# Kernel tuning notes

Hardware: AMD Instinct MI355X
Metric: run time of the kernel (lower is better)

The kernel has to match this reference:

```python
import jax, jax.numpy as jnp
import numpy as np

VOCAB = 50000
E = 256      # text_embed_dim
K = 512      # num_kernels
KS = 9       # kernel_size
L = 8192     # num labels
B, T = 8, 2048
PAD = KS // 2


def setup_inputs() -> dict:
    key = jax.random.key(0)
    ks = jax.random.split(key, 9)
    ids = jax.random.randint(ks[0], (B, T), 0, VOCAB)
    mask = jnp.ones((B, T), dtype=jnp.int32)  # unused by forward, kept for signature parity
    target = (jax.random.uniform(ks[1], (B, L)) < 0.01).astype(jnp.float32)
    embed_w = jax.random.normal(ks[2], (VOCAB, E), jnp.float32) * 0.02
    conv_w = jax.random.normal(ks[3], (K, E, KS), jnp.float32) * (1.0 / np.sqrt(E * KS))
    conv_b = jnp.zeros((K,), jnp.float32)
    U_w = jax.random.normal(ks[4], (L, K), jnp.float32) * (1.0 / np.sqrt(K))
    final_w = jax.random.normal(ks[5], (L, K), jnp.float32) * (1.0 / np.sqrt(K))
    final_b = jnp.zeros((L,), jnp.float32)
    return {"ids": ids, "mask": mask, "G": 0, "target": target,
            "embed_w": embed_w, "conv_w": conv_w, "conv_b": conv_b,
            "U_w": U_w, "final_w": final_w, "final_b": final_b}


def _forward(ids, embed_w, conv_w, conv_b, U_w, final_w, final_b):
    # embed + (dropout=identity in eval) -> [B, E, T]
    x = embed_w[ids].transpose(0, 2, 1)
    # same-padded Conv1d, then ReLU -> text_feats [B, T, K]
    y = jax.lax.conv_general_dilated(x, conv_w, (1,), [(PAD, PAD)],
                                     dimension_numbers=("NCH", "OIH", "NCH"))
    feats = jax.nn.relu(y + conv_b[None, :, None]).transpose(0, 2, 1)
    # label-wise attention: alpha = softmax(U.weight @ feats^T, dim=2) -> [B, L, T]
    scores = jnp.einsum("lk,btk->blt", U_w, feats)
    alpha = jax.nn.softmax(scores, axis=2)
    # attended features per label -> [B, L, K]
    attn = jnp.einsum("blt,btk->blk", alpha, feats)
    # label-wise dot with final.weight + bias -> logits [B, L]
    yhat = jnp.einsum("blk,lk->bl", attn, final_w) + final_b
    return yhat


def _bce_with_logits(yhat, target):
    # mean over all elements, numerically stable
    return jnp.mean(jnp.maximum(yhat, 0) - yhat * target + jnp.log1p(jnp.exp(-jnp.abs(yhat))))


def reference(ids, mask, G, target, embed_w, conv_w, conv_b, U_w, final_w, final_b):
    yhat = _forward(ids, embed_w, conv_w, conv_b, U_w, final_w, final_b)
    loss = _bce_with_logits(yhat, target)
    return yhat, loss
```

## Files before the change

### kernel.cpp

```cpp
#include <hip/hip_runtime.h>
#include <hip/hip_bf16.h>
#include <cstdint>

#define B_ 8
#define T_ 2048
#define E_ 256
#define K_ 512
#define KS_ 9
#define L_ 8192
#define PAD_ 4
#define TP_ (T_ + 2 * PAD_)
#define KK_ (E_ * KS_)

#define FEAT_SCALE 64.0f
#define W_SCALE 16.0f
#define INV_SS 9.765625e-4f
#define INV_SS_LOG2E 1.40888719e-3f

#define NB_EMBED ((B_ * TP_ * 64) / 256)
#define NB_WT ((K_ * KK_) / 256)
#define NB_CAST ((2 * L_ * K_ / 8) / 256)

typedef __bf16 bf16x8 __attribute__((ext_vector_type(8)));
typedef float f32x4 __attribute__((ext_vector_type(4)));
typedef float f32x16 __attribute__((ext_vector_type(16)));
typedef int i32x4 __attribute__((ext_vector_type(4)));
typedef int i32x8 __attribute__((ext_vector_type(8)));

__device__ __forceinline__ unsigned short f2bf(float f) {
  union { float f; unsigned int u; } a; a.f = f;
  unsigned int r = (a.u + 0x7FFFu + ((a.u >> 16) & 1u)) >> 16;
  return (unsigned short)r;
}

__device__ __forceinline__ unsigned char f2fp8(float v) {
  return (unsigned char)(__builtin_amdgcn_cvt_pk_fp8_f32(v, v, 0, false) & 0xFF);
}

__device__ __forceinline__ unsigned int pk4_fp8(float a, float b, float c, float d) {
  int v = __builtin_amdgcn_cvt_pk_fp8_f32(a, b, 0, false);
  v = __builtin_amdgcn_cvt_pk_fp8_f32(c, d, v, true);
  return (unsigned int)v;
}

__device__ __forceinline__ void gld_lds16(const void* g, void* l) {
  __builtin_amdgcn_global_load_lds(
      (const __attribute__((address_space(1))) unsigned int*)g,
      (__attribute__((address_space(3))) unsigned int*)l, 16, 0, 0);
}

__device__ __forceinline__ f32x4 mfma_bf16(bf16x8 a, bf16x8 b, f32x4 c) {
  return __builtin_amdgcn_mfma_f32_16x16x32_bf16(a, b, c, 0, 0, 0);
}

__device__ __forceinline__ f32x16 mfma_sc64(i32x8 a, i32x8 b, f32x16 c) {
  return __builtin_amdgcn_mfma_scale_f32_32x32x64_f8f6f4(a, b, c, 0, 0, 0, 127, 0, 127);
}

__device__ __forceinline__ int f_off(int t, int k) {
  return ((t >> 6) * 32768) + (((k >> 4) * 64 + (t & 63)) << 4) + (k & 15);
}
__device__ __forceinline__ int w_off(int l, int k) {
  return ((l >> 7) * 65536) + (((k >> 4) * 128 + (l & 127)) << 4) + (k & 15);
}

__global__ __launch_bounds__(256) void k_prep(const int* __restrict__ ids,
                                              const float* __restrict__ emb,
                                              const float* __restrict__ conv_w,
                                              const float* __restrict__ U_w,
                                              const float* __restrict__ F_w,
                                              unsigned short* __restrict__ xpad,
                                              unsigned short* __restrict__ wt,
                                              unsigned char* __restrict__ u8,
                                              unsigned char* __restrict__ f8) {
  const int bx = blockIdx.x;
  const int tid = threadIdx.x;
  if (bx < NB_EMBED) {
    int gid = bx * 256 + tid;
    int row = gid >> 6;
    int e4 = (gid & 63) << 2;
    int b = row / TP_;
    int tp = row - b * TP_;
    float4 v = make_float4(0.f, 0.f, 0.f, 0.f);
    if (tp >= PAD_ && tp < T_ + PAD_) {
      int id = ids[b * T_ + tp - PAD_];
      v = *(const float4*)(emb + (size_t)id * E_ + e4);
    }
    ushort4 o;
    o.x = f2bf(v.x); o.y = f2bf(v.y); o.z = f2bf(v.z); o.w = f2bf(v.w);
    *(ushort4*)(xpad + (size_t)row * E_ + e4) = o;
  } else if (bx < NB_EMBED + NB_WT) {
    int g = (bx - NB_EMBED) * 256 + tid;
    int k = g / KK_;
    int kk = g - k * KK_;
    int j = kk >> 8, e = kk & 255;
    wt[(size_t)k * KK_ + kk] = f2bf(conv_w[(k * E_ + e) * KS_ + j]);
  } else {
    int g = (bx - NB_EMBED - NB_WT) * 256 + tid;
    int sel = g >> 19;
    int gid = g & ((1 << 19) - 1);
    const float* src = sel ? F_w : U_w;
    unsigned char* dst = sel ? f8 : u8;
    int l = gid >> 6;
    int k0 = (gid & 63) << 3;
    const float* s = src + (size_t)l * K_ + k0;
    float4 v0 = *(const float4*)(s);
    float4 v1 = *(const float4*)(s + 4);
    uint2 o;
    o.x = pk4_fp8(v0.x * W_SCALE, v0.y * W_SCALE, v0.z * W_SCALE, v0.w * W_SCALE);
    o.y = pk4_fp8(v1.x * W_SCALE, v1.y * W_SCALE, v1.z * W_SCALE, v1.w * W_SCALE);
    *(uint2*)(dst + w_off(l, k0)) = o;
  }
}

__global__ __launch_bounds__(512, 4) void k_conv(const unsigned short* __restrict__ xpad,
                                                 const unsigned short* __restrict__ wt,
                                                 const float* __restrict__ conv_b,
                                                 unsigned char* __restrict__ feats) {
  __shared__ char At[2][16384];
  __shared__ char Bt[2][16384];
  const int tid = threadIdx.x;
  const int lane = tid & 63;
  const int q = lane >> 4, c = lane & 15;
  const int w = tid >> 6;
  const int wi = w >> 1, wj = w & 1;
  const int b = blockIdx.z;
  const int t0 = blockIdx.y * 128;
  const int n0 = blockIdx.x * 128;

  const char* xb = (const char*)(xpad + (size_t)b * TP_ * E_);
  const char* wb = (const char*)wt;

  const char* asrc[2]; const char* bsrc[2]; int ldso[2];
#pragma unroll
  for (int rnd = 0; rnd < 2; ++rnd) {
    int u = rnd * 512 + tid;
    int r = u >> 3;
    int j = (u & 7) ^ (r & 7);
    asrc[rnd] = xb + (size_t)(t0 + r) * 512 + j * 16;
    bsrc[rnd] = wb + (size_t)(n0 + r) * (KK_ * 2) + j * 16;
    ldso[rnd] = u * 16;
  }

  int offA[2][2], offB[4][2];
#pragma unroll
  for (int li = 0; li < 2; ++li) {
    int r = wi * 32 + li * 16 + c;
#pragma unroll
    for (int h = 0; h < 2; ++h) offA[li][h] = r * 128 + (((4 * h + q) ^ (r & 7)) << 4);
  }
#pragma unroll
  for (int ti = 0; ti < 4; ++ti) {
    int r = wj * 64 + ti * 16 + c;
#pragma unroll
    for (int h = 0; h < 2; ++h) offB[ti][h] = r * 128 + (((4 * h + q) ^ (r & 7)) << 4);
  }

  f32x4 acc[2][4];
  f32x4 zero = {0.f, 0.f, 0.f, 0.f};
#pragma unroll
  for (int i = 0; i < 2; ++i)
#pragma unroll
    for (int j = 0; j < 4; ++j) acc[i][j] = zero;

#pragma unroll
  for (int rnd = 0; rnd < 2; ++rnd) {
    gld_lds16(asrc[rnd], At[0] + ldso[rnd]);
    gld_lds16(bsrc[rnd], Bt[0] + ldso[rnd]);
  }

  for (int it = 0; it < 36; ++it) {
    const int bsel = it & 1;
    __syncthreads();
    if (it != 35) {
      const int kkc = (it + 1) * 64;
      const int aofs = (kkc >> 8) * 512 + (kkc & 255) * 2;
      const int bofs = kkc * 2;
#pragma unroll
      for (int rnd = 0; rnd < 2; ++rnd) {
        gld_lds16(asrc[rnd] + aofs, At[bsel ^ 1] + ldso[rnd]);
        gld_lds16(bsrc[rnd] + bofs, Bt[bsel ^ 1] + ldso[rnd]);
      }
    }
    const char* aB = At[bsel];
    const char* bB = Bt[bsel];
#pragma unroll
    for (int h = 0; h < 2; ++h) {
      bf16x8 afr[2], bfr[4];
#pragma unroll
      for (int li = 0; li < 2; ++li) afr[li] = *(const bf16x8*)(aB + offA[li][h]);
#pragma unroll
      for (int ti = 0; ti < 4; ++ti) bfr[ti] = *(const bf16x8*)(bB + offB[ti][h]);
#pragma unroll
      for (int ti = 0; ti < 4; ++ti)
#pragma unroll
        for (int li = 0; li < 2; ++li)
          acc[li][ti] = mfma_bf16(afr[li], bfr[ti], acc[li][ti]);
    }
  }

  const size_t fbase = (size_t)b * T_ * K_;
#pragma unroll
  for (int ti = 0; ti < 4; ++ti) {
    int k = n0 + wj * 64 + ti * 16 + c;
    float bias = conv_b[k];
#pragma unroll
    for (int li = 0; li < 2; ++li) {
      int tb = t0 + wi * 32 + li * 16 + q * 4;
#pragma unroll
      for (int rr = 0; rr < 4; ++rr) {
        float v = fmaxf(acc[li][ti][rr] + bias, 0.f) * FEAT_SCALE;
        int t = tb + rr;
        feats[fbase + f_off(t, k)] = f2fp8(v);
      }
    }
  }
}

__global__ __launch_bounds__(512, 2) void k_attn(const unsigned char* __restrict__ feats,
                                                 const unsigned char* __restrict__ u8,
                                                 const unsigned char* __restrict__ f8,
                                                 const float* __restrict__ final_b,
                                                 float* __restrict__ out) {
  __shared__ __align__(16) char smem[131072];
  __shared__ float red[512];
  const int tid = threadIdx.x;
  const int lane = tid & 63;
  const int q2 = lane >> 5, c32 = lane & 31;
  const int w = tid >> 6;
  const int wi = w >> 1;
  const int wj = w & 1;
  const int b = blockIdx.y;
  const int l0 = blockIdx.x * 128;

  const unsigned char* fb = feats + (size_t)b * T_ * K_;

  char* Us = smem;
  char* Ws = smem + 65536;
#pragma unroll
  for (int rr = 0; rr < 8; ++rr) {
    gld_lds16(u8 + (size_t)l0 * K_ + rr * 8192 + tid * 16, Us + rr * 8192 + tid * 16);
    gld_lds16(f8 + (size_t)l0 * K_ + rr * 8192 + tid * 16, Ws + rr * 8192 + tid * 16);
  }
  __syncthreads();

  const int arow = wi * 32 + c32;
  const int abase = q2 * 4096 + arow * 16;
  i32x8 uf[8], wf[8];
#pragma unroll
  for (int s = 0; s < 8; ++s) {
    int o0 = abase + s * 8192;
    i32x4 ul = *(const i32x4*)(Us + o0);
    i32x4 uh = *(const i32x4*)(Us + o0 + 2048);
    i32x4 wl = *(const i32x4*)(Ws + o0);
    i32x4 wh = *(const i32x4*)(Ws + o0 + 2048);
    uf[s] = __builtin_shufflevector(ul, uh, 0, 1, 2, 3, 4, 5, 6, 7);
    wf[s] = __builtin_shufflevector(wl, wh, 0, 1, 2, 3, 4, 5, 6, 7);
  }
  __syncthreads();

  char* const Fs0 = smem;
  char* const Fs1 = smem + 32768;
  const unsigned char* fsrc = fb + tid * 16;
#pragma unroll
  for (int rr = 0; rr < 4; ++rr)
    gld_lds16(fsrc + rr * 8192, Fs0 + tid * 16 + rr * 8192);

  const int brow = wj * 32 + c32;
  const int bbase = q2 * 2048 + brow * 16;

  f32x16 zc;
#pragma unroll
  for (int r = 0; r < 16; ++r) zc[r] = 0.f;

  float num[16], den[16];
#pragma unroll
  for (int r = 0; r < 16; ++r) { num[r] = 0.f; den[r] = 0.f; }

  for (int tc = 0; tc < 32; ++tc) {
    const int bsel = tc & 1;
    char* const cur = bsel ? Fs1 : Fs0;
    char* const nxt = bsel ? Fs0 : Fs1;
    __syncthreads();
    if (tc != 31) {
      const unsigned char* nsrc = fsrc + (size_t)(tc + 1) * 32768;
#pragma unroll
      for (int rr = 0; rr < 4; ++rr)
        gld_lds16(nsrc + rr * 8192, nxt + tid * 16 + rr * 8192);
    }
    f32x16 accS, accV;
    {
      i32x4 flo = *(const i32x4*)(cur + bbase);
      i32x4 fhi = *(const i32x4*)(cur + bbase + 1024);
      i32x8 fa = __builtin_shufflevector(flo, fhi, 0, 1, 2, 3, 4, 5, 6, 7);
      accS = mfma_sc64(uf[0], fa, zc);
      accV = mfma_sc64(wf[0], fa, zc);
    }
#pragma unroll
    for (int s = 1; s < 8; ++s) {
      i32x4 flo = *(const i32x4*)(cur + bbase + s * 4096);
      i32x4 fhi = *(const i32x4*)(cur + bbase + s * 4096 + 1024);
      i32x8 fa = __builtin_shufflevector(flo, fhi, 0, 1, 2, 3, 4, 5, 6, 7);
      accS = mfma_sc64(uf[s], fa, accS);
      accV = mfma_sc64(wf[s], fa, accV);
    }
#pragma unroll
    for (int r = 0; r < 16; ++r) {
      float p = __builtin_exp2f(accS[r] * INV_SS_LOG2E);
      den[r] += p;
      num[r] += p * accV[r];
    }
  }

#pragma unroll
  for (int r = 0; r < 16; ++r) {
#pragma unroll
    for (int m = 1; m < 32; m <<= 1) {
      num[r] += __shfl_xor(num[r], m, 64);
      den[r] += __shfl_xor(den[r], m, 64);
    }
  }
  if (c32 == 0) {
#pragma unroll
    for (int r = 0; r < 16; ++r) {
      int ll = wi * 32 + (r & 3) + 8 * (r >> 2) + 4 * q2;
      red[wj * 256 + ll] = num[r];
      red[wj * 256 + 128 + ll] = den[r];
    }
  }
  __syncthreads();
  if (tid < 128) {
    int l = l0 + tid;
    float n = red[tid] + red[256 + tid];
    float d = red[128 + tid] + red[384 + tid];
    out[(size_t)b * L_ + l] = (n * INV_SS) / d + final_b[l];
  }
}

__global__ __launch_bounds__(256) void k_loss(const float* __restrict__ yhat,
                                              const float* __restrict__ target,
                                              float* __restrict__ loss) {
  int gid = blockIdx.x * 256 + threadIdx.x;
  float s = 0.f;
  for (int i = gid; i < B_ * L_; i += 64 * 256) {
    float y = yhat[i], t = target[i];
    s += fmaxf(y, 0.f) - y * t + log1pf(__expf(-fabsf(y)));
  }
#pragma unroll
  for (int m = 1; m < 64; m <<= 1) s += __shfl_xor(s, m, 64);
  if ((threadIdx.x & 63) == 0) atomicAdd(loss, s * (1.0f / (B_ * L_)));
}

extern "C" void kernel_launch(void* const* d_in, const int* in_sizes, int n_in,
                              void* d_out, int out_size, void* d_ws, size_t ws_size,
                              hipStream_t stream) {
  const int* ids = (const int*)d_in[0];
  const float* target = (const float*)d_in[3];
  const float* emb = (const float*)d_in[4];
  const float* conv_w = (const float*)d_in[5];
  const float* conv_b = (const float*)d_in[6];
  const float* U_w = (const float*)d_in[7];
  const float* F_w = (const float*)d_in[8];
  const float* final_b = (const float*)d_in[9];
  float* out = (float*)d_out;

  char* ws = (char*)d_ws;
  unsigned short* xpad = (unsigned short*)ws;
  size_t off = (size_t)B_ * TP_ * E_ * 2;
  unsigned short* wt = (unsigned short*)(ws + off);
  off += (size_t)K_ * KK_ * 2;
  unsigned char* u8 = (unsigned char*)(ws + off);
  off += (size_t)L_ * K_;
  unsigned char* f8 = (unsigned char*)(ws + off);
  off += (size_t)L_ * K_;
  unsigned char* feats = (unsigned char*)(ws + off);
  off += (size_t)B_ * T_ * K_;
  if (ws_size < off) return;

  k_prep<<<dim3(NB_EMBED + NB_WT + NB_CAST), 256, 0, stream>>>(
      ids, emb, conv_w, U_w, F_w, xpad, wt, u8, f8);
  hipMemsetAsync(out + B_ * L_, 0, sizeof(float), stream);
  k_conv<<<dim3(K_ / 128, T_ / 128, B_), 512, 0, stream>>>(xpad, wt, conv_b, feats);
  k_attn<<<dim3(L_ / 128, B_), 512, 0, stream>>>(feats, u8, f8, final_b, out);
  k_loss<<<dim3(64), 256, 0, stream>>>(out, target, out + B_ * L_);
}
```

Baseline: 289.4 us.

## Rework conv GEMM to 32x32x16 MFMA with 256-thread blocks and new LDS layout

The conv GEMM kernel now uses 32x32x16 bf16 MFMA instead of 16x16x32. It runs 4 waves per block, each computing a 64x64 tile with four 32x32 accumulators, and the LDS staging is laid out k-major in 16-byte column chunks rather than XOR-swizzled rows. The fp8 weight cast in prep now writes 16-byte chunks per thread instead of 8. The attention kernel zeroes its accumulators in place rather than special-casing the first MFMA. The aim is fewer LDS reads per MFMA and wider stores. The risks are LDS bank conflicts from the new unswizzled layout and lower occupancy per block.

```diff
diff --git a/kernel.cpp b/kernel.cpp
--- a/kernel.cpp
+++ b/kernel.cpp
@@ -19,7 +19,7 @@
 
 #define NB_EMBED ((B_ * TP_ * 64) / 256)
 #define NB_WT ((K_ * KK_) / 256)
-#define NB_CAST ((2 * L_ * K_ / 8) / 256)
+#define NB_CAST 2048
 
 typedef __bf16 bf16x8 __attribute__((ext_vector_type(8)));
 typedef float f32x4 __attribute__((ext_vector_type(4)));
@@ -49,8 +49,8 @@
       (__attribute__((address_space(3))) unsigned int*)l, 16, 0, 0);
 }
 
-__device__ __forceinline__ f32x4 mfma_bf16(bf16x8 a, bf16x8 b, f32x4 c) {
-  return __builtin_amdgcn_mfma_f32_16x16x32_bf16(a, b, c, 0, 0, 0);
+__device__ __forceinline__ f32x16 mfma32_bf16(bf16x8 a, bf16x8 b, f32x16 c) {
+  return __builtin_amdgcn_mfma_f32_32x32x16_bf16(a, b, c, 0, 0, 0);
 }
 
 __device__ __forceinline__ f32x16 mfma_sc64(i32x8 a, i32x8 b, f32x16 c) {
@@ -97,33 +97,37 @@
     wt[(size_t)k * KK_ + kk] = f2bf(conv_w[(k * E_ + e) * KS_ + j]);
   } else {
     int g = (bx - NB_EMBED - NB_WT) * 256 + tid;
-    int sel = g >> 19;
-    int gid = g & ((1 << 19) - 1);
+    int sel = g >> 18;
+    int gi = g & ((1 << 18) - 1);
+    int u = (gi >> 6) & 31;
+    int l = ((gi >> 11) << 6) | (gi & 63);
     const float* src = sel ? F_w : U_w;
     unsigned char* dst = sel ? f8 : u8;
-    int l = gid >> 6;
-    int k0 = (gid & 63) << 3;
-    const float* s = src + (size_t)l * K_ + k0;
+    const float* s = src + (size_t)l * K_ + u * 16;
     float4 v0 = *(const float4*)(s);
     float4 v1 = *(const float4*)(s + 4);
-    uint2 o;
+    float4 v2 = *(const float4*)(s + 8);
+    float4 v3 = *(const float4*)(s + 12);
+    uint4 o;
     o.x = pk4_fp8(v0.x * W_SCALE, v0.y * W_SCALE, v0.z * W_SCALE, v0.w * W_SCALE);
     o.y = pk4_fp8(v1.x * W_SCALE, v1.y * W_SCALE, v1.z * W_SCALE, v1.w * W_SCALE);
-    *(uint2*)(dst + w_off(l, k0)) = o;
-  }
-}
-
-__global__ __launch_bounds__(512, 4) void k_conv(const unsigned short* __restrict__ xpad,
+    o.z = pk4_fp8(v2.x * W_SCALE, v2.y * W_SCALE, v2.z * W_SCALE, v2.w * W_SCALE);
+    o.w = pk4_fp8(v3.x * W_SCALE, v3.y * W_SCALE, v3.z * W_SCALE, v3.w * W_SCALE);
+    *(uint4*)(dst + w_off(l, u * 16)) = o;
+  }
+}
+
+__global__ __launch_bounds__(256, 2) void k_conv(const unsigned short* __restrict__ xpad,
                                                  const unsigned short* __restrict__ wt,
                                                  const float* __restrict__ conv_b,
                                                  unsigned char* __restrict__ feats) {
-  __shared__ char At[2][16384];
-  __shared__ char Bt[2][16384];
+  __shared__ __align__(16) char sm[2][32768];
   const int tid = threadIdx.x;
   const int lane = tid & 63;
-  const int q = lane >> 4, c = lane & 15;
+  const int q2 = lane >> 5, c32 = lane & 31;
   const int w = tid >> 6;
-  const int wi = w >> 1, wj = w & 1;
+  const int wt_i = w >> 1;
+  const int wn = w & 1;
   const int b = blockIdx.z;
   const int t0 = blockIdx.y * 128;
   const int n0 = blockIdx.x * 128;
@@ -131,90 +135,75 @@
   const char* xb = (const char*)(xpad + (size_t)b * TP_ * E_);
   const char* wb = (const char*)wt;
 
-  const char* asrc[2]; const char* bsrc[2]; int ldso[2];
-#pragma unroll
-  for (int rnd = 0; rnd < 2; ++rnd) {
-    int u = rnd * 512 + tid;
-    int r = u >> 3;
-    int j = (u & 7) ^ (r & 7);
-    asrc[rnd] = xb + (size_t)(t0 + r) * 512 + j * 16;
-    bsrc[rnd] = wb + (size_t)(n0 + r) * (KK_ * 2) + j * 16;
-    ldso[rnd] = u * 16;
-  }
-
-  int offA[2][2], offB[4][2];
-#pragma unroll
-  for (int li = 0; li < 2; ++li) {
-    int r = wi * 32 + li * 16 + c;
-#pragma unroll
-    for (int h = 0; h < 2; ++h) offA[li][h] = r * 128 + (((4 * h + q) ^ (r & 7)) << 4);
-  }
-#pragma unroll
-  for (int ti = 0; ti < 4; ++ti) {
-    int r = wj * 64 + ti * 16 + c;
-#pragma unroll
-    for (int h = 0; h < 2; ++h) offB[ti][h] = r * 128 + (((4 * h + q) ^ (r & 7)) << 4);
-  }
-
-  f32x4 acc[2][4];
-  f32x4 zero = {0.f, 0.f, 0.f, 0.f};
-#pragma unroll
-  for (int i = 0; i < 2; ++i)
-#pragma unroll
-    for (int j = 0; j < 4; ++j) acc[i][j] = zero;
-
-#pragma unroll
-  for (int rnd = 0; rnd < 2; ++rnd) {
-    gld_lds16(asrc[rnd], At[0] + ldso[rnd]);
-    gld_lds16(bsrc[rnd], Bt[0] + ldso[rnd]);
-  }
+  const char* aptr[4]; int au8[4];
+  const char* bptr[4];
+#pragma unroll
+  for (int r = 0; r < 4; ++r) {
+    int d = r * 4096 + tid * 16;
+    int u = d >> 11;
+    int row = (d >> 4) & 127;
+    aptr[r] = xb + (size_t)(t0 + row) * 512;
+    au8[r] = u * 8;
+    bptr[r] = wb + (size_t)(n0 + row) * (KK_ * 2) + u * 16;
+  }
+  const int ldso = tid * 16;
+
+#define STAGE(BUF, KKC)                                                    \
+  {                                                                        \
+    _Pragma("unroll") for (int r = 0; r < 4; ++r) {                        \
+      int kkg = (KKC) + au8[r];                                            \
+      int j = kkg >> 8, e0 = kkg & 255;                                    \
+      gld_lds16(aptr[r] + j * 512 + e0 * 2, (BUF) + r * 4096 + ldso);      \
+    }                                                                      \
+    _Pragma("unroll") for (int r = 0; r < 4; ++r)                          \
+      gld_lds16(bptr[r] + (KKC) * 2, (BUF) + 16384 + r * 4096 + ldso);     \
+  }
+
+  f32x16 acc00, acc01, acc10, acc11;
+#pragma unroll
+  for (int r = 0; r < 16; ++r) { acc00[r] = 0.f; acc01[r] = 0.f; acc10[r] = 0.f; acc11[r] = 0.f; }
+
+  STAGE(sm[0], 0)
+
+  const int aoff0 = (wt_i * 64 + c32) * 16;
+  const int boff0 = 16384 + (wn * 64 + c32) * 16;
 
   for (int it = 0; it < 36; ++it) {
-    const int bsel = it & 1;
     __syncthreads();
-    if (it != 35) {
-      const int kkc = (it + 1) * 64;
-      const int aofs = (kkc >> 8) * 512 + (kkc & 255) * 2;
-      const int bofs = kkc * 2;
-#pragma unroll
-      for (int rnd = 0; rnd < 2; ++rnd) {
-        gld_lds16(asrc[rnd] + aofs, At[bsel ^ 1] + ldso[rnd]);
-        gld_lds16(bsrc[rnd] + bofs, Bt[bsel ^ 1] + ldso[rnd]);
-      }
-    }
-    const char* aB = At[bsel];
-    const char* bB = Bt[bsel];
-#pragma unroll
-    for (int h = 0; h < 2; ++h) {
-      bf16x8 afr[2], bfr[4];
-#pragma unroll
-      for (int li = 0; li < 2; ++li) afr[li] = *(const bf16x8*)(aB + offA[li][h]);
-#pragma unroll
-      for (int ti = 0; ti < 4; ++ti) bfr[ti] = *(const bf16x8*)(bB + offB[ti][h]);
-#pragma unroll
-      for (int ti = 0; ti < 4; ++ti)
-#pragma unroll
-        for (int li = 0; li < 2; ++li)
-          acc[li][ti] = mfma_bf16(afr[li], bfr[ti], acc[li][ti]);
-    }
-  }
+    if (it != 35) STAGE(sm[(it + 1) & 1], (it + 1) * 64)
+    const char* buf = sm[it & 1];
+#pragma unroll
+    for (int ks = 0; ks < 4; ++ks) {
+      const char* base = buf + (ks * 2 + q2) * 2048;
+      bf16x8 a0 = *(const bf16x8*)(base + aoff0);
+      bf16x8 a1 = *(const bf16x8*)(base + aoff0 + 512);
+      bf16x8 b0 = *(const bf16x8*)(base + boff0);
+      bf16x8 b1 = *(const bf16x8*)(base + boff0 + 512);
+      acc00 = mfma32_bf16(a0, b0, acc00);
+      acc01 = mfma32_bf16(a0, b1, acc01);
+      acc10 = mfma32_bf16(a1, b0, acc10);
+      acc11 = mfma32_bf16(a1, b1, acc11);
+    }
+  }
+#undef STAGE
 
   const size_t fbase = (size_t)b * T_ * K_;
-#pragma unroll
-  for (int ti = 0; ti < 4; ++ti) {
-    int k = n0 + wj * 64 + ti * 16 + c;
-    float bias = conv_b[k];
-#pragma unroll
-    for (int li = 0; li < 2; ++li) {
-      int tb = t0 + wi * 32 + li * 16 + q * 4;
-#pragma unroll
-      for (int rr = 0; rr < 4; ++rr) {
-        float v = fmaxf(acc[li][ti][rr] + bias, 0.f) * FEAT_SCALE;
-        int t = tb + rr;
-        feats[fbase + f_off(t, k)] = f2fp8(v);
-      }
-    }
-  }
+  const float bias0 = conv_b[n0 + wn * 64 + c32];
+  const float bias1 = conv_b[n0 + wn * 64 + 32 + c32];
+#define EPI(ACC, TA, TB, BIAS)                                              \
+  {                                                                         \
+    _Pragma("unroll") for (int r = 0; r < 16; ++r) {                        \
+      int trow = t0 + wt_i * 64 + (TA) * 32 + (r & 3) + 8 * (r >> 2) + 4 * q2; \
+      int k = n0 + wn * 64 + (TB) * 32 + c32;                               \
+      float v = fmaxf(ACC[r] + (BIAS), 0.f) * FEAT_SCALE;                   \
+      feats[fbase + f_off(trow, k)] = f2fp8(v);                             \
+    }                                                                       \
+  }
+  EPI(acc00, 0, 0, bias0)
+  EPI(acc01, 0, 1, bias1)
+  EPI(acc10, 1, 0, bias0)
+  EPI(acc11, 1, 1, bias1)
+#undef EPI
 }
 
 __global__ __launch_bounds__(512, 2) void k_attn(const unsigned char* __restrict__ feats,
@@ -269,13 +258,10 @@
   const int brow = wj * 32 + c32;
   const int bbase = q2 * 2048 + brow * 16;
 
-  f32x16 zc;
-#pragma unroll
-  for (int r = 0; r < 16; ++r) zc[r] = 0.f;
-
+  f32x16 accS, accV;
   float num[16], den[16];
 #pragma unroll
-  for (int r = 0; r < 16; ++r) { num[r] = 0.f; den[r] = 0.f; }
+  for (int r = 0; r < 16; ++r) { accS[r] = 0.f; accV[r] = 0.f; num[r] = 0.f; den[r] = 0.f; }
 
   for (int tc = 0; tc < 32; ++tc) {
     const int bsel = tc & 1;
@@ -288,16 +274,8 @@
       for (int rr = 0; rr < 4; ++rr)
         gld_lds16(nsrc + rr * 8192, nxt + tid * 16 + rr * 8192);
     }
-    f32x16 accS, accV;
-    {
-      i32x4 flo = *(const i32x4*)(cur + bbase);
-      i32x4 fhi = *(const i32x4*)(cur + bbase + 1024);
-      i32x8 fa = __builtin_shufflevector(flo, fhi, 0, 1, 2, 3, 4, 5, 6, 7);
-      accS = mfma_sc64(uf[0], fa, zc);
-      accV = mfma_sc64(wf[0], fa, zc);
-    }
-#pragma unroll
-    for (int s = 1; s < 8; ++s) {
+#pragma unroll
+    for (int s = 0; s < 8; ++s) {
       i32x4 flo = *(const i32x4*)(cur + bbase + s * 4096);
       i32x4 fhi = *(const i32x4*)(cur + bbase + s * 4096 + 1024);
       i32x8 fa = __builtin_shufflevector(flo, fhi, 0, 1, 2, 3, 4, 5, 6, 7);
@@ -309,6 +287,8 @@
       float p = __builtin_exp2f(accS[r] * INV_SS_LOG2E);
       den[r] += p;
       num[r] += p * accV[r];
+      accS[r] = 0.f;
+      accV[r] = 0.f;
     }
   }
 
@@ -380,7 +360,7 @@
   k_prep<<<dim3(NB_EMBED + NB_WT + NB_CAST), 256, 0, stream>>>(
       ids, emb, conv_w, U_w, F_w, xpad, wt, u8, f8);
   hipMemsetAsync(out + B_ * L_, 0, sizeof(float), stream);
-  k_conv<<<dim3(K_ / 128, T_ / 128, B_), 512, 0, stream>>>(xpad, wt, conv_b, feats);
+  k_conv<<<dim3(K_ / 128, T_ / 128, B_), 256, 0, stream>>>(xpad, wt, conv_b, feats);
   k_attn<<<dim3(L_ / 128, B_), 512, 0, stream>>>(feats, u8, f8, final_b, out);
   k_loss<<<dim3(64), 256, 0, stream>>>(out, target, out + B_ * L_);
 }
```

New measurement: 326.0 us. +12.7%, slower.
